# Kernel tuning notes

Hardware: AMD Instinct MI355X
Metric: run time of the kernel (lower is better)

The kernel has to match this reference:

```python
import jax, jax.numpy as jnp
import numpy as np

T, B, E, H, L, V = 256, 64, 512, 1024, 2, 32000
PAD = 0


def _lstm_scan(x, mask, Wih, Whh, bih, bhh, reverse):
    # x: [T, B, I], mask: [T, B, 1] bool. torch.nn.LSTMCell math, packed-seq
    # semantics: inactive (padded) rows keep previous state and emit zeros.
    Bsz = x.shape[1]
    Hs = Whh.shape[1]
    h0 = jnp.zeros((Bsz, Hs), x.dtype)
    c0 = jnp.zeros((Bsz, Hs), x.dtype)

    def step(carry, inp):
        h, c = carry
        xt, mt = inp
        gates = xt @ Wih.T + bih + h @ Whh.T + bhh  # [B, 4H]
        i, f, g, o = jnp.split(gates, 4, axis=-1)
        i = jax.nn.sigmoid(i)
        f = jax.nn.sigmoid(f)
        g = jnp.tanh(g)
        o = jax.nn.sigmoid(o)
        c2 = f * c + i * g
        h2 = o * jnp.tanh(c2)
        h = jnp.where(mt, h2, h)
        c = jnp.where(mt, c2, c)
        out = jnp.where(mt, h2, jnp.zeros((), x.dtype))
        return (h, c), out

    _, outs = jax.lax.scan(step, (h0, c0), (x, mask), reverse=reverse)
    return outs  # [T, B, H]


def _elmo_dir(x, mask, layers, reverse):
    outs = []
    for l, (Wih, Whh, bih, bhh) in enumerate(layers):
        y = _lstm_scan(x, mask, Wih, Whh, bih, bhh, reverse)
        if l != 0:
            y = y + x  # residual between stacked layers (l != 0)
        outs.append(y)
        x = y
    return jnp.stack(outs, axis=-2)  # [T, B, L, H]


def setup_inputs() -> dict:
    key = jax.random.key(0)
    ks = jax.random.split(key, 8)
    lens = jnp.sort(jax.random.randint(ks[0], (B,), 1, T + 1))[::-1]
    lens = lens.at[0].set(T)  # pack_padded_sequence requires descending lens, max = T
    input_ids = jax.random.randint(ks[1], (T, B), 0, V)
    embed = (jax.random.normal(ks[2], (V, E), dtype=jnp.float32) * 0.05).at[PAD].set(0.0)
    s = 1.0 / float(np.sqrt(H))

    def cell(k, I):
        k1, k2, k3, k4 = jax.random.split(k, 4)
        return (jax.random.uniform(k1, (4 * H, I), minval=-s, maxval=s),
                jax.random.uniform(k2, (4 * H, H), minval=-s, maxval=s),
                jax.random.uniform(k3, (4 * H,), minval=-s, maxval=s),
                jax.random.uniform(k4, (4 * H,), minval=-s, maxval=s))

    d = {"input_ids": input_ids, "lens": lens, "embed": embed}
    for name, k, I in (("fw0", ks[3], E), ("fw1", ks[4], H), ("bw0", ks[5], E), ("bw1", ks[6], H)):
        Wih, Whh, bih, bhh = cell(k, I)
        d[name + "_Wih"], d[name + "_Whh"], d[name + "_bih"], d[name + "_bhh"] = Wih, Whh, bih, bhh
    return d


def reference(input_ids, lens, embed,
              fw0_Wih, fw0_Whh, fw0_bih, fw0_bhh,
              fw1_Wih, fw1_Whh, fw1_bih, fw1_bhh,
              bw0_Wih, bw0_Whh, bw0_bih, bw0_bhh,
              bw1_Wih, bw1_Whh, bw1_bih, bw1_bhh):
    mask = (jnp.arange(T)[:, None] < lens[None, :])[..., None]  # [T, B, 1]
    x = embed[input_ids]  # [T, B, E]
    fwd_layers = [(fw0_Wih, fw0_Whh, fw0_bih, fw0_bhh), (fw1_Wih, fw1_Whh, fw1_bih, fw1_bhh)]
    bwd_layers = [(bw0_Wih, bw0_Whh, bw0_bih, bw0_bhh), (bw1_Wih, bw1_Whh, bw1_bih, bw1_bhh)]
    fwd = _elmo_dir(x, mask, fwd_layers, reverse=False)  # [T, B, L, H]
    bwd = _elmo_dir(x, mask, bwd_layers, reverse=True)   # [T, B, L, H]
    return jnp.stack([fwd, bwd], axis=0)  # [2, T, B, L, H]
```

## Files before the change

kernel.cpp:

```cpp
#include <hip/hip_runtime.h>
#include <stdint.h>

#define TT 256
#define BB 64
#define EE 512
#define HH 1024

typedef short s8v __attribute__((ext_vector_type(8)));
typedef float f4v __attribute__((ext_vector_type(4)));
typedef unsigned short u16;

static __device__ __forceinline__ u16 f2bf(float f) {
  uint32_t u = __float_as_uint(f);
  return (u16)((u + 0x7fffu + ((u >> 16) & 1u)) >> 16);
}
static __device__ __forceinline__ float bf2f(u16 b) {
  return __uint_as_float(((uint32_t)b) << 16);
}

struct P {
  const int* ids; const int* lens; const float* emb;
  const float* bih[2][2]; const float* bhh[2][2];
  const u16* W[2][2][2];
  float* out;
  float* h[2];
  u16* hpl[2];
  float* c[2];
  u16* y0pl;
};

__global__ void prep_w(const float* Wih, const float* Whh, int KX, int K,
                       u16* dH, u16* dM) {
  const size_t total = (size_t)128 * K * 32;
  for (size_t idx = (size_t)blockIdx.x * 256 + threadIdx.x; idx < total;
       idx += (size_t)gridDim.x * 256) {
    const int c = (int)(idx & 31);
    const int k = (int)((idx >> 5) % K);
    const int jb = (int)(idx / ((size_t)K * 32));
    const int n = (c >> 3) * HH + jb * 8 + (c & 7);
    const float v = (k < KX) ? Wih[(size_t)n * KX + k] : Whh[(size_t)n * HH + (k - KX)];
    const u16 h = f2bf(v);
    const u16 m = f2bf(v - bf2f(h));
    const size_t off = ((size_t)jb * (K / 32) + (k >> 5)) * 1024 +
                       ((k >> 3) & 3) * 256 + c * 8 + (k & 7);
    dH[off] = h; dM[off] = m;
  }
}

template <int LAYER, int K, int KX, int NST>
static __device__ __forceinline__ void run_layer(const P& p, int s, int ub,
                                                 u16 (*lds)[8192], float* epi) {
  const int tid = threadIdx.x;
  const int w = tid >> 6, l = tid & 63, lr = l & 15, kgq = l >> 4;
  const int unit = ub >> 7;
  const int jb = ub & 127;
  const int dir = unit;
  const int t = dir ? (TT - 1 - s) : s;
  const int row = w * 16 + lr;

  const u16* WH = p.W[LAYER][unit][0] + (size_t)jb * (K / 32) * 1024;
  const u16* WM = p.W[LAYER][unit][1] + (size_t)jb * (K / 32) * 1024;
  const uint4* gH = (const uint4*)WH;
  const uint4* gM = (const uint4*)WM;

  const u16* hp2 = p.hpl[LAYER] + (size_t)((((s - 1) & 1) * 2 + unit) * 2) * BB * HH;
  const u16* y2  = p.y0pl + (size_t)(((s & 1) * 2 + unit) * 2) * BB * HH;
  const float* xsrc = nullptr;
  if (LAYER == 0) {
    const int id = p.ids[t * BB + row];
    xsrc = p.emb + (size_t)id * EE;
  }

  f4v acc[2];
  { f4v z = {0.f, 0.f, 0.f, 0.f}; acc[0] = z; acc[1] = z; }

  uint4 rH[4], rM[4];
#pragma unroll
  for (int i = 0; i < 4; ++i) { rH[i] = gH[i * 256 + tid]; rM[i] = gM[i * 256 + tid]; }
  {
    uint4* dH = (uint4*)lds[0]; uint4* dM = (uint4*)lds[1];
#pragma unroll
    for (int i = 0; i < 4; ++i) { dH[i * 256 + tid] = rH[i]; dM[i * 256 + tid] = rM[i]; }
  }
  __syncthreads();

  int cur = 0;
  for (int q = 0; q < NST; ++q) {
    if (q + 1 < NST) {
#pragma unroll
      for (int i = 0; i < 4; ++i) {
        rH[i] = gH[(size_t)(q + 1) * 1024 + i * 256 + tid];
        rM[i] = gM[(size_t)(q + 1) * 1024 + i * 256 + tid];
      }
    }
    const u16* lH = lds[cur * 2 + 0];
    const u16* lM = lds[cur * 2 + 1];
    for (int ktl = 0; ktl < 8; ++ktl) {
      const int ktg = q * 8 + ktl;
      const int k0 = ktg * 32 + kgq * 8;
      s8v a0, a1;
      if (LAYER == 0 && k0 < KX) {
        const float4 f0 = *(const float4*)(xsrc + k0);
        const float4 f1 = *(const float4*)(xsrc + k0 + 4);
        const float tf[8] = {f0.x, f0.y, f0.z, f0.w, f1.x, f1.y, f1.z, f1.w};
#pragma unroll
        for (int e = 0; e < 8; ++e) {
          const u16 hh = f2bf(tf[e]);
          a0[e] = (short)hh;
          a1[e] = (short)f2bf(tf[e] - bf2f(hh));
        }
      } else if (LAYER == 1 && k0 < KX) {
        const size_t o = (size_t)row * HH + k0;
        a0 = *(const s8v*)(y2 + o);
        a1 = *(const s8v*)(y2 + (size_t)BB * HH + o);
      } else {
        if (s == 0) continue;
        const size_t o = (size_t)row * HH + (k0 - KX);
        a0 = *(const s8v*)(hp2 + o);
        a1 = *(const s8v*)(hp2 + (size_t)BB * HH + o);
      }
#pragma unroll
      for (int ct = 0; ct < 2; ++ct) {
        const int bo = ((ktl * 4 + kgq) * 32 + ct * 16 + lr) * 8;
        const s8v bh = *(const s8v*)(lH + bo);
        const s8v bm = *(const s8v*)(lM + bo);
        acc[ct] = __builtin_amdgcn_mfma_f32_16x16x32_bf16(a0, bh, acc[ct], 0, 0, 0);
        acc[ct] = __builtin_amdgcn_mfma_f32_16x16x32_bf16(a0, bm, acc[ct], 0, 0, 0);
        acc[ct] = __builtin_amdgcn_mfma_f32_16x16x32_bf16(a1, bh, acc[ct], 0, 0, 0);
      }
    }
    if (q + 1 < NST) {
      uint4* dH = (uint4*)lds[(cur ^ 1) * 2 + 0];
      uint4* dM = (uint4*)lds[(cur ^ 1) * 2 + 1];
#pragma unroll
      for (int i = 0; i < 4; ++i) { dH[i * 256 + tid] = rH[i]; dM[i * 256 + tid] = rM[i]; }
    }
    __syncthreads();
    cur ^= 1;
  }

#pragma unroll
  for (int ct = 0; ct < 2; ++ct)
#pragma unroll
    for (int qq = 0; qq < 4; ++qq)
      epi[(w * 32 + ct * 16 + lr) * 17 + kgq * 4 + qq] = acc[ct][qq];
  __syncthreads();

  const float* bi = p.bih[LAYER][unit];
  const float* bh_ = p.bhh[LAYER][unit];
  float* hF = p.h[LAYER] + (size_t)((s & 1) * 2 + unit) * BB * HH;
  const float* hFp = p.h[LAYER] + (size_t)(((s - 1) & 1) * 2 + unit) * BB * HH;
  u16* hPl = p.hpl[LAYER] + (size_t)(((s & 1) * 2 + unit) * 2) * BB * HH;
  float* cS = p.c[LAYER] + (size_t)unit * BB * HH;
  u16* yPl = p.y0pl + (size_t)(((s & 1) * 2 + unit) * 2) * BB * HH;

#pragma unroll
  for (int oi2 = 0; oi2 < 2; ++oi2) {
    const int oi = l + oi2 * 64;
    const int r = oi >> 3, jj = oi & 7;
    const int rg = w * 16 + r;
    const int j = jb * 8 + jj;
    float g4[4];
#pragma unroll
    for (int g = 0; g < 4; ++g)
      g4[g] = epi[(w * 32 + g * 8 + jj) * 17 + r] + bi[g * HH + j] + bh_[g * HH + j];
    const bool m = (t < p.lens[rg]);
    const size_t hx = (size_t)rg * HH + j;
    const float c0 = (s > 0) ? cS[hx] : 0.f;
    const float iv = 1.f / (1.f + expf(-g4[0]));
    const float fv = 1.f / (1.f + expf(-g4[1]));
    const float gv = tanhf(g4[2]);
    const float ov = 1.f / (1.f + expf(-g4[3]));
    const float cn = fv * c0 + iv * gv;
    const float hn = ov * tanhf(cn);
    cS[hx] = m ? cn : c0;
    const float hp0 = (s > 0) ? hFp[hx] : 0.f;
    const float hc = m ? hn : hp0;
    hF[hx] = hc;
    const u16 h1 = f2bf(hc);
    const u16 h2 = f2bf(hc - bf2f(h1));
    hPl[hx] = h1;
    hPl[(size_t)BB * HH + hx] = h2;
    const size_t orow = ((size_t)(dir * TT + t) * BB + rg) * (2 * HH);
    if (LAYER == 0) {
      const float y = m ? hn : 0.f;
      p.out[orow + j] = y;
      const u16 y1 = f2bf(y);
      const u16 ylo = f2bf(y - bf2f(y1));
      yPl[hx] = y1;
      yPl[(size_t)BB * HH + hx] = ylo;
    } else {
      const float y0v = p.out[orow + j];
      p.out[orow + HH + j] = m ? (hn + y0v) : 0.f;
    }
  }
}

__global__ __launch_bounds__(256, 2) void step_fused(P p, int sd) {
  __shared__ __align__(16) u16 lds[4][8192];
  __shared__ float epi[4 * 32 * 17];
  const int bid = blockIdx.x;
  if (bid < 256) {
    if (sd < TT) run_layer<0, 1536, 512, 6>(p, sd, bid, lds, epi);
  } else {
    if (sd >= 1) run_layer<1, 2048, 1024, 8>(p, sd - 1, bid - 256, lds, epi);
  }
}

extern "C" void kernel_launch(void* const* d_in, const int* in_sizes, int n_in,
                              void* d_out, int out_size, void* d_ws, size_t ws_size,
                              hipStream_t stream) {
  if (n_in != 19) return;
  if (in_sizes[0] != TT * BB || in_sizes[1] != BB) return;
  if (in_sizes[2] != 32000 * EE) return;
  if (in_sizes[3] != 4 * HH * EE || in_sizes[4] != 4 * HH * HH) return;
  if (in_sizes[7] != 4 * HH * HH || in_sizes[8] != 4 * HH * HH) return;
  if (in_sizes[11] != 4 * HH * EE || in_sizes[15] != 4 * HH * HH) return;
  if (out_size != 2 * TT * BB * 2 * HH) return;
  if (ws_size < 123731968u) return;

  char* ws = (char*)d_ws;
  u16* WA = (u16*)ws;
  u16* WB = (u16*)(ws + 50331648);
  float* hA = (float*)(ws + 117440512);
  u16* hApl = (u16*)(ws + 118489088);
  float* cA = (float*)(ws + 119537664);
  float* hB = (float*)(ws + 120061952);
  u16* hBpl = (u16*)(ws + 121110528);
  float* cB = (float*)(ws + 122159104);
  u16* y0pl = (u16*)(ws + 122683392);

  P p;
  p.ids = (const int*)d_in[0];
  p.lens = (const int*)d_in[1];
  p.emb = (const float*)d_in[2];
  const float* WihA[2] = {(const float*)d_in[3], (const float*)d_in[11]};
  const float* WhhA[2] = {(const float*)d_in[4], (const float*)d_in[12]};
  p.bih[0][0] = (const float*)d_in[5];  p.bhh[0][0] = (const float*)d_in[6];
  p.bih[0][1] = (const float*)d_in[13]; p.bhh[0][1] = (const float*)d_in[14];
  const float* WihB[2] = {(const float*)d_in[7], (const float*)d_in[15]};
  const float* WhhB[2] = {(const float*)d_in[8], (const float*)d_in[16]};
  p.bih[1][0] = (const float*)d_in[9];  p.bhh[1][0] = (const float*)d_in[10];
  p.bih[1][1] = (const float*)d_in[17]; p.bhh[1][1] = (const float*)d_in[18];
  for (int u = 0; u < 2; ++u) {
    p.W[0][u][0] = WA + (size_t)(u * 2 + 0) * 6291456;
    p.W[0][u][1] = WA + (size_t)(u * 2 + 1) * 6291456;
    p.W[1][u][0] = WB + (size_t)(u * 2 + 0) * 8388608;
    p.W[1][u][1] = WB + (size_t)(u * 2 + 1) * 8388608;
  }
  p.out = (float*)d_out;
  p.h[0] = hA; p.h[1] = hB;
  p.hpl[0] = hApl; p.hpl[1] = hBpl;
  p.c[0] = cA; p.c[1] = cB;
  p.y0pl = y0pl;

  for (int u = 0; u < 2; ++u) {
    prep_w<<<4096, 256, 0, stream>>>(WihA[u], WhhA[u], EE, 1536,
                                     (u16*)p.W[0][u][0], (u16*)p.W[0][u][1]);
    prep_w<<<4096, 256, 0, stream>>>(WihB[u], WhhB[u], HH, 2048,
                                     (u16*)p.W[1][u][0], (u16*)p.W[1][u][1]);
  }
  for (int sd = 0; sd <= TT; ++sd)
    step_fused<<<512, 256, 0, stream>>>(p, sd);
}
```

Baseline: 13.59 ms.

## Replace per-step launches with persistent cooperative kernel keeping weights in registers and LDS

The 257 per-timestep kernel launches become one cooperative persistent kernel of 256 blocks. Each block runs both layer 0 and layer 1 for one column slice in two 256-thread halves, and the halves are kept in lockstep by a global atomic barrier spun on by thread 0 each step. The bf16 hi/mid weight fragments are loaded once into registers and LDS rather than restreamed from global memory every step, which removes launch overhead and repeated weight traffic. In exchange it carries high register pressure, a barrier that spins with a timeout, and a dependence on all blocks being co-resident.

```diff
diff --git a/kernel.cpp b/kernel.cpp
--- a/kernel.cpp
+++ b/kernel.cpp
@@ -5,6 +5,8 @@
 #define BB 64
 #define EE 512
 #define HH 1024
+#define RLX __ATOMIC_RELAXED
+#define AGT __HIP_MEMORY_SCOPE_AGENT
 
 typedef short s8v __attribute__((ext_vector_type(8)));
 typedef float f4v __attribute__((ext_vector_type(4)));
@@ -17,16 +19,27 @@
 static __device__ __forceinline__ float bf2f(u16 b) {
   return __uint_as_float(((uint32_t)b) << 16);
 }
+static __device__ __forceinline__ void split8(const float4 f0, const float4 f1,
+                                              s8v& a0, s8v& a1) {
+  const float tf[8] = {f0.x, f0.y, f0.z, f0.w, f1.x, f1.y, f1.z, f1.w};
+#pragma unroll
+  for (int e = 0; e < 8; ++e) {
+    const u16 h = f2bf(tf[e]);
+    a0[e] = (short)h;
+    a1[e] = (short)f2bf(tf[e] - bf2f(h));
+  }
+}
+#define MFMA __builtin_amdgcn_mfma_f32_16x16x32_bf16
 
 struct P {
   const int* ids; const int* lens; const float* emb;
   const float* bih[2][2]; const float* bhh[2][2];
   const u16* W[2][2][2];
   float* out;
-  float* h[2];
-  u16* hpl[2];
-  float* c[2];
-  u16* y0pl;
+  u16 *h0pl, *y0pl, *h1pl;
+  float *hF0, *hF1;
+  float *c0, *c1;
+  uint32_t* bar;
 };
 
 __global__ void prep_w(const float* Wih, const float* Whh, int KX, int K,
@@ -47,163 +60,315 @@
   }
 }
 
-template <int LAYER, int K, int KX, int NST>
-static __device__ __forceinline__ void run_layer(const P& p, int s, int ub,
-                                                 u16 (*lds)[8192], float* epi) {
+__global__ void prep_zero_bar(uint32_t* bar) { if (threadIdx.x == 0) *bar = 0; }
+
+__global__ __launch_bounds__(512, 2) void elmo_persist(P p) {
+  __shared__ __align__(16) u16 ldsM0[16384];
+  __shared__ __align__(16) u16 ldsM1[49152];
+  __shared__ float epi[2][4][64][8];
   const int tid = threadIdx.x;
-  const int w = tid >> 6, l = tid & 63, lr = l & 15, kgq = l >> 4;
-  const int unit = ub >> 7;
-  const int jb = ub & 127;
+  const int wid = tid >> 6, l = tid & 63, lr = l & 15, kg = l >> 4;
+  const int g = wid >> 2, kq = wid & 3;
+  const int bid = blockIdx.x;
+  const int unit = bid >> 7, jb = bid & 127;
   const int dir = unit;
-  const int t = dir ? (TT - 1 - s) : s;
-  const int row = w * 16 + lr;
-
-  const u16* WH = p.W[LAYER][unit][0] + (size_t)jb * (K / 32) * 1024;
-  const u16* WM = p.W[LAYER][unit][1] + (size_t)jb * (K / 32) * 1024;
-  const uint4* gH = (const uint4*)WH;
-  const uint4* gM = (const uint4*)WM;
-
-  const u16* hp2 = p.hpl[LAYER] + (size_t)((((s - 1) & 1) * 2 + unit) * 2) * BB * HH;
-  const u16* y2  = p.y0pl + (size_t)(((s & 1) * 2 + unit) * 2) * BB * HH;
-  const float* xsrc = nullptr;
-  if (LAYER == 0) {
-    const int id = p.ids[t * BB + row];
-    xsrc = p.emb + (size_t)id * EE;
-  }
-
-  f4v acc[2];
-  { f4v z = {0.f, 0.f, 0.f, 0.f}; acc[0] = z; acc[1] = z; }
-
-  uint4 rH[4], rM[4];
-#pragma unroll
-  for (int i = 0; i < 4; ++i) { rH[i] = gH[i * 256 + tid]; rM[i] = gM[i * 256 + tid]; }
+  const size_t PL = 65536;
+
   {
-    uint4* dH = (uint4*)lds[0]; uint4* dM = (uint4*)lds[1];
-#pragma unroll
-    for (int i = 0; i < 4; ++i) { dH[i * 256 + tid] = rH[i]; dM[i * 256 + tid] = rM[i]; }
+    const uint4* s0 = (const uint4*)(p.W[0][unit][1] + (size_t)jb * 48 * 1024);
+    const uint4* s1 = (const uint4*)(p.W[1][unit][1] + (size_t)jb * 64 * 1024 + 16384);
+    uint4* d0 = (uint4*)ldsM0; uint4* d1 = (uint4*)ldsM1;
+    for (int i = tid; i < 2048; i += 512) d0[i] = s0[i];
+    for (int i = tid; i < 6144; i += 512) d1[i] = s1[i];
+  }
+  const int tg = tid - g * 256;
+  const int colp = (tg & 3) * 2;
+  const int jcol = jb * 8 + colp;
+  float bias2[4][2]; int len4[4];
+  if (tg < 64) {
+#pragma unroll
+    for (int gi = 0; gi < 4; ++gi)
+#pragma unroll
+      for (int uu = 0; uu < 2; ++uu)
+        bias2[gi][uu] = p.bih[g][unit][gi * HH + jcol + uu] +
+                        p.bhh[g][unit][gi * HH + jcol + uu];
+#pragma unroll
+    for (int rt = 0; rt < 4; ++rt) len4[rt] = p.lens[rt * 16 + (tg >> 2)];
   }
   __syncthreads();
 
-  int cur = 0;
-  for (int q = 0; q < NST; ++q) {
-    if (q + 1 < NST) {
-#pragma unroll
-      for (int i = 0; i < 4; ++i) {
-        rH[i] = gH[(size_t)(q + 1) * 1024 + i * 256 + tid];
-        rM[i] = gM[(size_t)(q + 1) * 1024 + i * 256 + tid];
+  if (g == 0) {
+    s8v wfh[12][2], wfm[8][2];
+    const u16* WH = p.W[0][unit][0] + (size_t)jb * 48 * 1024;
+    const u16* WM = p.W[0][unit][1] + (size_t)jb * 48 * 1024;
+#pragma unroll
+    for (int i = 0; i < 12; ++i) {
+      const int kt = kq + 4 * i;
+#pragma unroll
+      for (int ct = 0; ct < 2; ++ct)
+        wfh[i][ct] = *(const s8v*)(WH + kt * 1024 + kg * 256 + (ct * 16 + lr) * 8);
+    }
+#pragma unroll
+    for (int i = 0; i < 8; ++i) {
+      const int kt = kq + 4 * (i + 4);
+#pragma unroll
+      for (int ct = 0; ct < 2; ++ct)
+        wfm[i][ct] = *(const s8v*)(WM + kt * 1024 + kg * 256 + (ct * 16 + lr) * 8);
+    }
+    float* cS = p.c0 + (size_t)unit * PL;
+#pragma unroll 1
+    for (int it = 0; it <= TT; ++it) {
+      const int s = it;
+      const bool act = (s < TT);
+      const int t = dir ? (TT - 1 - s) : s;
+      f4v acc[4][2];
+#pragma unroll
+      for (int rt = 0; rt < 4; ++rt)
+#pragma unroll
+        for (int ct = 0; ct < 2; ++ct) { f4v z = {0.f,0.f,0.f,0.f}; acc[rt][ct] = z; }
+      if (act) {
+        int idr[4];
+#pragma unroll
+        for (int rt = 0; rt < 4; ++rt) idr[rt] = p.ids[t * BB + rt * 16 + lr];
+#pragma unroll
+        for (int i = 0; i < 4; ++i) {
+          const int kt = kq + 4 * i;
+          const int k0 = kt * 32 + kg * 8;
+#pragma unroll
+          for (int rt = 0; rt < 4; ++rt) {
+            const float* xs = p.emb + (size_t)idr[rt] * EE + k0;
+            s8v a0, a1;
+            split8(*(const float4*)xs, *(const float4*)(xs + 4), a0, a1);
+#pragma unroll
+            for (int ct = 0; ct < 2; ++ct) {
+              const s8v bm = *(const s8v*)(ldsM0 + kt * 1024 + kg * 256 + (ct * 16 + lr) * 8);
+              acc[rt][ct] = MFMA(a0, wfh[i][ct], acc[rt][ct], 0, 0, 0);
+              acc[rt][ct] = MFMA(a0, bm, acc[rt][ct], 0, 0, 0);
+              acc[rt][ct] = MFMA(a1, wfh[i][ct], acc[rt][ct], 0, 0, 0);
+            }
+          }
+        }
+        if (s > 0) {
+          const u16* hhi = p.h0pl + (((size_t)((s - 1) & 1) * 2 + unit) * 2) * PL;
+          const u16* hmi = hhi + PL;
+#pragma unroll
+          for (int i = 0; i < 8; ++i) {
+            const int kt = kq + 4 * (i + 4);
+            const int kh = (kt - 16) * 32 + kg * 8;
+#pragma unroll
+            for (int rt = 0; rt < 4; ++rt) {
+              const int row = rt * 16 + lr;
+              const s8v a0 = *(const s8v*)(hhi + (size_t)row * HH + kh);
+              const s8v a1 = *(const s8v*)(hmi + (size_t)row * HH + kh);
+#pragma unroll
+              for (int ct = 0; ct < 2; ++ct) {
+                acc[rt][ct] = MFMA(a0, wfh[i + 4][ct], acc[rt][ct], 0, 0, 0);
+                acc[rt][ct] = MFMA(a0, wfm[i][ct], acc[rt][ct], 0, 0, 0);
+                acc[rt][ct] = MFMA(a1, wfh[i + 4][ct], acc[rt][ct], 0, 0, 0);
+              }
+            }
+          }
+        }
       }
-    }
-    const u16* lH = lds[cur * 2 + 0];
-    const u16* lM = lds[cur * 2 + 1];
-    for (int ktl = 0; ktl < 8; ++ktl) {
-      const int ktg = q * 8 + ktl;
-      const int k0 = ktg * 32 + kgq * 8;
-      s8v a0, a1;
-      if (LAYER == 0 && k0 < KX) {
-        const float4 f0 = *(const float4*)(xsrc + k0);
-        const float4 f1 = *(const float4*)(xsrc + k0 + 4);
-        const float tf[8] = {f0.x, f0.y, f0.z, f0.w, f1.x, f1.y, f1.z, f1.w};
-#pragma unroll
-        for (int e = 0; e < 8; ++e) {
-          const u16 hh = f2bf(tf[e]);
-          a0[e] = (short)hh;
-          a1[e] = (short)f2bf(tf[e] - bf2f(hh));
-        }
-      } else if (LAYER == 1 && k0 < KX) {
-        const size_t o = (size_t)row * HH + k0;
-        a0 = *(const s8v*)(y2 + o);
-        a1 = *(const s8v*)(y2 + (size_t)BB * HH + o);
-      } else {
-        if (s == 0) continue;
-        const size_t o = (size_t)row * HH + (k0 - KX);
-        a0 = *(const s8v*)(hp2 + o);
-        a1 = *(const s8v*)(hp2 + (size_t)BB * HH + o);
+      u16* h0hiC = p.h0pl + (((size_t)(s & 1) * 2 + unit) * 2) * PL;
+      u16* h0miC = h0hiC + PL;
+      u16* y0hiC = p.y0pl + (((size_t)(s & 1) * 2 + unit) * 2) * PL;
+      u16* y0miC = y0hiC + PL;
+      float* hFc = p.hF0 + ((size_t)(s & 1) * 2 + unit) * PL;
+      const float* hFp = p.hF0 + ((size_t)((s - 1) & 1) * 2 + unit) * PL;
+      for (int rt = 0; rt < 4; ++rt) {
+        if (act) {
+          *(f4v*)&epi[0][kq][l][0] = acc[rt][0];
+          *(f4v*)&epi[0][kq][l][4] = acc[rt][1];
+        }
+        __syncthreads();
+        if (act && tg < 64) {
+          const int rowin = tg >> 2;
+          const int row = rt * 16 + rowin;
+          const int kgc = rowin >> 2, qc = rowin & 3;
+          const bool m = (t < len4[rt]);
+          float outv[2]; u16 hh2[2], hm2[2], yh2[2], ym2[2];
+#pragma unroll
+          for (int uu = 0; uu < 2; ++uu) {
+            float g4[4];
+#pragma unroll
+            for (int gi = 0; gi < 4; ++gi) {
+              const int c = gi * 8 + colp + uu;
+              const int lrc = c & 15, ctc = c >> 4;
+              float ssum = bias2[gi][uu];
+#pragma unroll
+              for (int k = 0; k < 4; ++k) ssum += epi[0][k][kgc * 16 + lrc][ctc * 4 + qc];
+              g4[gi] = ssum;
+            }
+            const size_t hx = (size_t)row * HH + jcol + uu;
+            const float c0v = (s > 0) ? cS[hx] : 0.f;
+            const float iv = 1.f / (1.f + expf(-g4[0]));
+            const float fv = 1.f / (1.f + expf(-g4[1]));
+            const float gv = tanhf(g4[2]);
+            const float ov = 1.f / (1.f + expf(-g4[3]));
+            const float cn = fv * c0v + iv * gv;
+            const float hn = ov * tanhf(cn);
+            cS[hx] = m ? cn : c0v;
+            const float hp0 = (s > 0) ? hFp[hx] : 0.f;
+            const float hc = m ? hn : hp0;
+            hFc[hx] = hc;
+            hh2[uu] = f2bf(hc); hm2[uu] = f2bf(hc - bf2f(hh2[uu]));
+            const float y = m ? hn : 0.f;
+            outv[uu] = y;
+            yh2[uu] = f2bf(y); ym2[uu] = f2bf(y - bf2f(yh2[uu]));
+          }
+          const size_t orow = ((size_t)(dir * TT + t) * BB + row) * (2 * HH);
+          p.out[orow + jcol] = outv[0];
+          p.out[orow + jcol + 1] = outv[1];
+          const size_t px = (size_t)row * HH + jcol;
+          __hip_atomic_store((uint32_t*)(h0hiC + px), (uint32_t)hh2[0] | ((uint32_t)hh2[1] << 16), RLX, AGT);
+          __hip_atomic_store((uint32_t*)(h0miC + px), (uint32_t)hm2[0] | ((uint32_t)hm2[1] << 16), RLX, AGT);
+          __hip_atomic_store((uint32_t*)(y0hiC + px), (uint32_t)yh2[0] | ((uint32_t)yh2[1] << 16), RLX, AGT);
+          __hip_atomic_store((uint32_t*)(y0miC + px), (uint32_t)ym2[0] | ((uint32_t)ym2[1] << 16), RLX, AGT);
+        }
+        __syncthreads();
       }
-#pragma unroll
-      for (int ct = 0; ct < 2; ++ct) {
-        const int bo = ((ktl * 4 + kgq) * 32 + ct * 16 + lr) * 8;
-        const s8v bh = *(const s8v*)(lH + bo);
-        const s8v bm = *(const s8v*)(lM + bo);
-        acc[ct] = __builtin_amdgcn_mfma_f32_16x16x32_bf16(a0, bh, acc[ct], 0, 0, 0);
-        acc[ct] = __builtin_amdgcn_mfma_f32_16x16x32_bf16(a0, bm, acc[ct], 0, 0, 0);
-        acc[ct] = __builtin_amdgcn_mfma_f32_16x16x32_bf16(a1, bh, acc[ct], 0, 0, 0);
+      __syncthreads();
+      if (tid == 0) {
+        __builtin_amdgcn_fence(__ATOMIC_RELEASE, "agent");
+        __hip_atomic_fetch_add(p.bar, 1u, RLX, AGT);
+        const uint32_t tgt = 256u * (uint32_t)(it + 1);
+        int gd = 0;
+        while (__hip_atomic_load(p.bar, RLX, AGT) < tgt && gd < (1 << 22)) {
+          __builtin_amdgcn_s_sleep(8); ++gd;
+        }
+        __builtin_amdgcn_fence(__ATOMIC_ACQUIRE, "agent");
       }
-    }
-    if (q + 1 < NST) {
-      uint4* dH = (uint4*)lds[(cur ^ 1) * 2 + 0];
-      uint4* dM = (uint4*)lds[(cur ^ 1) * 2 + 1];
-#pragma unroll
-      for (int i = 0; i < 4; ++i) { dH[i * 256 + tid] = rH[i]; dM[i * 256 + tid] = rM[i]; }
-    }
-    __syncthreads();
-    cur ^= 1;
-  }
-
-#pragma unroll
-  for (int ct = 0; ct < 2; ++ct)
-#pragma unroll
-    for (int qq = 0; qq < 4; ++qq)
-      epi[(w * 32 + ct * 16 + lr) * 17 + kgq * 4 + qq] = acc[ct][qq];
-  __syncthreads();
-
-  const float* bi = p.bih[LAYER][unit];
-  const float* bh_ = p.bhh[LAYER][unit];
-  float* hF = p.h[LAYER] + (size_t)((s & 1) * 2 + unit) * BB * HH;
-  const float* hFp = p.h[LAYER] + (size_t)(((s - 1) & 1) * 2 + unit) * BB * HH;
-  u16* hPl = p.hpl[LAYER] + (size_t)(((s & 1) * 2 + unit) * 2) * BB * HH;
-  float* cS = p.c[LAYER] + (size_t)unit * BB * HH;
-  u16* yPl = p.y0pl + (size_t)(((s & 1) * 2 + unit) * 2) * BB * HH;
-
-#pragma unroll
-  for (int oi2 = 0; oi2 < 2; ++oi2) {
-    const int oi = l + oi2 * 64;
-    const int r = oi >> 3, jj = oi & 7;
-    const int rg = w * 16 + r;
-    const int j = jb * 8 + jj;
-    float g4[4];
-#pragma unroll
-    for (int g = 0; g < 4; ++g)
-      g4[g] = epi[(w * 32 + g * 8 + jj) * 17 + r] + bi[g * HH + j] + bh_[g * HH + j];
-    const bool m = (t < p.lens[rg]);
-    const size_t hx = (size_t)rg * HH + j;
-    const float c0 = (s > 0) ? cS[hx] : 0.f;
-    const float iv = 1.f / (1.f + expf(-g4[0]));
-    const float fv = 1.f / (1.f + expf(-g4[1]));
-    const float gv = tanhf(g4[2]);
-    const float ov = 1.f / (1.f + expf(-g4[3]));
-    const float cn = fv * c0 + iv * gv;
-    const float hn = ov * tanhf(cn);
-    cS[hx] = m ? cn : c0;
-    const float hp0 = (s > 0) ? hFp[hx] : 0.f;
-    const float hc = m ? hn : hp0;
-    hF[hx] = hc;
-    const u16 h1 = f2bf(hc);
-    const u16 h2 = f2bf(hc - bf2f(h1));
-    hPl[hx] = h1;
-    hPl[(size_t)BB * HH + hx] = h2;
-    const size_t orow = ((size_t)(dir * TT + t) * BB + rg) * (2 * HH);
-    if (LAYER == 0) {
-      const float y = m ? hn : 0.f;
-      p.out[orow + j] = y;
-      const u16 y1 = f2bf(y);
-      const u16 ylo = f2bf(y - bf2f(y1));
-      yPl[hx] = y1;
-      yPl[(size_t)BB * HH + hx] = ylo;
-    } else {
-      const float y0v = p.out[orow + j];
-      p.out[orow + HH + j] = m ? (hn + y0v) : 0.f;
-    }
-  }
-}
-
-__global__ __launch_bounds__(256, 2) void step_fused(P p, int sd) {
-  __shared__ __align__(16) u16 lds[4][8192];
-  __shared__ float epi[4 * 32 * 17];
-  const int bid = blockIdx.x;
-  if (bid < 256) {
-    if (sd < TT) run_layer<0, 1536, 512, 6>(p, sd, bid, lds, epi);
+      __syncthreads();
+    }
   } else {
-    if (sd >= 1) run_layer<1, 2048, 1024, 8>(p, sd - 1, bid - 256, lds, epi);
+    s8v wfh[16][2], wfm[4][2];
+    const u16* WH = p.W[1][unit][0] + (size_t)jb * 64 * 1024;
+    const u16* WM = p.W[1][unit][1] + (size_t)jb * 64 * 1024;
+#pragma unroll
+    for (int i = 0; i < 16; ++i) {
+      const int kt = kq + 4 * i;
+#pragma unroll
+      for (int ct = 0; ct < 2; ++ct)
+        wfh[i][ct] = *(const s8v*)(WH + kt * 1024 + kg * 256 + (ct * 16 + lr) * 8);
+    }
+#pragma unroll
+    for (int i = 0; i < 4; ++i) {
+      const int kt = kq + 4 * i;
+#pragma unroll
+      for (int ct = 0; ct < 2; ++ct)
+        wfm[i][ct] = *(const s8v*)(WM + kt * 1024 + kg * 256 + (ct * 16 + lr) * 8);
+    }
+    float* cS = p.c1 + (size_t)unit * PL;
+#pragma unroll 1
+    for (int it = 0; it <= TT; ++it) {
+      const int u = it - 1;
+      const bool act = (it >= 1);
+      const int t = dir ? (TT - 1 - u) : u;
+      f4v acc[4][2];
+#pragma unroll
+      for (int rt = 0; rt < 4; ++rt)
+#pragma unroll
+        for (int ct = 0; ct < 2; ++ct) { f4v z = {0.f,0.f,0.f,0.f}; acc[rt][ct] = z; }
+      if (act) {
+        const u16* yhi = p.y0pl + (((size_t)(u & 1) * 2 + unit) * 2) * PL;
+        const u16* ymi = yhi + PL;
+#pragma unroll
+        for (int i = 0; i < 8; ++i) {
+          const int kt = kq + 4 * i;
+          const int k0 = kt * 32 + kg * 8;
+#pragma unroll
+          for (int rt = 0; rt < 4; ++rt) {
+            const int row = rt * 16 + lr;
+            const s8v a0 = *(const s8v*)(yhi + (size_t)row * HH + k0);
+            const s8v a1 = *(const s8v*)(ymi + (size_t)row * HH + k0);
+#pragma unroll
+            for (int ct = 0; ct < 2; ++ct) {
+              const s8v bm = (i < 4) ? wfm[i & 3][ct]
+                  : *(const s8v*)(ldsM1 + (kt - 16) * 1024 + kg * 256 + (ct * 16 + lr) * 8);
+              acc[rt][ct] = MFMA(a0, wfh[i][ct], acc[rt][ct], 0, 0, 0);
+              acc[rt][ct] = MFMA(a0, bm, acc[rt][ct], 0, 0, 0);
+              acc[rt][ct] = MFMA(a1, wfh[i][ct], acc[rt][ct], 0, 0, 0);
+            }
+          }
+        }
+        if (u > 0) {
+          const u16* hhi = p.h1pl + (((size_t)((u - 1) & 1) * 2 + unit) * 2) * PL;
+          const u16* hmi = hhi + PL;
+#pragma unroll
+          for (int i = 8; i < 16; ++i) {
+            const int kt = kq + 4 * i;
+            const int kh = (kt - 32) * 32 + kg * 8;
+#pragma unroll
+            for (int rt = 0; rt < 4; ++rt) {
+              const int row = rt * 16 + lr;
+              const s8v a0 = *(const s8v*)(hhi + (size_t)row * HH + kh);
+              const s8v a1 = *(const s8v*)(hmi + (size_t)row * HH + kh);
+#pragma unroll
+              for (int ct = 0; ct < 2; ++ct) {
+                const s8v bm = *(const s8v*)(ldsM1 + (kt - 16) * 1024 + kg * 256 + (ct * 16 + lr) * 8);
+                acc[rt][ct] = MFMA(a0, wfh[i][ct], acc[rt][ct], 0, 0, 0);
+                acc[rt][ct] = MFMA(a0, bm, acc[rt][ct], 0, 0, 0);
+                acc[rt][ct] = MFMA(a1, wfh[i][ct], acc[rt][ct], 0, 0, 0);
+              }
+            }
+          }
+        }
+      }
+      u16* h1hiC = p.h1pl + (((size_t)(u & 1) * 2 + unit) * 2) * PL;
+      u16* h1miC = h1hiC + PL;
+      float* hFc = p.hF1 + ((size_t)(u & 1) * 2 + unit) * PL;
+      const float* hFp = p.hF1 + ((size_t)((u - 1) & 1) * 2 + unit) * PL;
+      for (int rt = 0; rt < 4; ++rt) {
+        if (act) {
+          *(f4v*)&epi[1][kq][l][0] = acc[rt][0];
+          *(f4v*)&epi[1][kq][l][4] = acc[rt][1];
+        }
+        __syncthreads();
+        if (act && tg < 64) {
+          const int rowin = tg >> 2;
+          const int row = rt * 16 + rowin;
+          const int kgc = rowin >> 2, qc = rowin & 3;
+          const bool m = (t < len4[rt]);
+          const size_t orow = ((size_t)(dir * TT + t) * BB + row) * (2 * HH);
+          u16 hh2[2], hm2[2];
+#pragma unroll
+          for (int uu = 0; uu < 2; ++uu) {
+            float g4[4];
+#pragma unroll
+            for (int gi = 0; gi < 4; ++gi) {
+              const int c = gi * 8 + colp + uu;
+              const int lrc = c & 15, ctc = c >> 4;
+              float ssum = bias2[gi][uu];
+#pragma unroll
+              for (int k = 0; k < 4; ++k) ssum += epi[1][k][kgc * 16 + lrc][ctc * 4 + qc];
+              g4[gi] = ssum;
+            }
+            const size_t hx = (size_t)row * HH + jcol + uu;
+            const float c0v = (u > 0) ? cS[hx] : 0.f;
+            const float iv = 1.f / (1.f + expf(-g4[0]));
+            const float fv = 1.f / (1.f + expf(-g4[1]));
+            const float gv = tanhf(g4[2]);
+            const float ov = 1.f / (1.f + expf(-g4[3]));
+            const float cn = fv * c0v + iv * gv;
+            const float hn = ov * tanhf(cn);
+            cS[hx] = m ? cn : c0v;
+            const float hp0 = (u > 0) ? hFp[hx] : 0.f;
+            const float hc = m ? hn : hp0;
+            hFc[hx] = hc;
+            hh2[uu] = f2bf(hc); hm2[uu] = f2bf(hc - bf2f(hh2[uu]));
+            const float y0v = p.out[orow + jcol + uu];
+            p.out[orow + HH + jcol + uu] = m ? (hn + y0v) : 0.f;
+          }
+          const size_t px = (size_t)row * HH + jcol;
+          __hip_atomic_store((uint32_t*)(h1hiC + px), (uint32_t)hh2[0] | ((uint32_t)hh2[1] << 16), RLX, AGT);
+          __hip_atomic_store((uint32_t*)(h1miC + px), (uint32_t)hm2[0] | ((uint32_t)hm2[1] << 16), RLX, AGT);
+        }
+        __syncthreads();
+      }
+      __syncthreads();
+      __syncthreads();
+    }
   }
 }
 
@@ -217,18 +382,19 @@
   if (in_sizes[7] != 4 * HH * HH || in_sizes[8] != 4 * HH * HH) return;
   if (in_sizes[11] != 4 * HH * EE || in_sizes[15] != 4 * HH * HH) return;
   if (out_size != 2 * TT * BB * 2 * HH) return;
-  if (ws_size < 123731968u) return;
+  if (ws_size < 128974976u) return;
 
   char* ws = (char*)d_ws;
   u16* WA = (u16*)ws;
   u16* WB = (u16*)(ws + 50331648);
-  float* hA = (float*)(ws + 117440512);
-  u16* hApl = (u16*)(ws + 118489088);
-  float* cA = (float*)(ws + 119537664);
-  float* hB = (float*)(ws + 120061952);
-  u16* hBpl = (u16*)(ws + 121110528);
-  float* cB = (float*)(ws + 122159104);
-  u16* y0pl = (u16*)(ws + 122683392);
+  u16* h0pl = (u16*)(ws + 117440512);
+  u16* y0pl = (u16*)(ws + 119537664);
+  u16* h1pl = (u16*)(ws + 121634816);
+  float* hF0 = (float*)(ws + 123731968);
+  float* hF1 = (float*)(ws + 125829120);
+  float* c0  = (float*)(ws + 127926272);
+  float* c1  = (float*)(ws + 128450560);
+  uint32_t* bar = (uint32_t*)(ws + 128974848);
 
   P p;
   p.ids = (const int*)d_in[0];
@@ -249,10 +415,9 @@
     p.W[1][u][1] = WB + (size_t)(u * 2 + 1) * 8388608;
   }
   p.out = (float*)d_out;
-  p.h[0] = hA; p.h[1] = hB;
-  p.hpl[0] = hApl; p.hpl[1] = hBpl;
-  p.c[0] = cA; p.c[1] = cB;
-  p.y0pl = y0pl;
+  p.h0pl = h0pl; p.y0pl = y0pl; p.h1pl = h1pl;
+  p.hF0 = hF0; p.hF1 = hF1; p.c0 = c0; p.c1 = c1;
+  p.bar = bar;
 
   for (int u = 0; u < 2; ++u) {
     prep_w<<<4096, 256, 0, stream>>>(WihA[u], WhhA[u], EE, 1536,
@@ -260,6 +425,8 @@
     prep_w<<<4096, 256, 0, stream>>>(WihB[u], WhhB[u], HH, 2048,
                                      (u16*)p.W[1][u][0], (u16*)p.W[1][u][1]);
   }
-  for (int sd = 0; sd <= TT; ++sd)
-    step_fused<<<512, 256, 0, stream>>>(p, sd);
-}
+  prep_zero_bar<<<1, 64, 0, stream>>>(bar);
+  void* kargs[] = {&p};
+  hipLaunchCooperativeKernel(reinterpret_cast<void*>(&elmo_persist),
+                             dim3(256), dim3(512), kargs, 0, stream);
+}
```

Result: slower. 15.63 ms (+15.0%).
